# Performance work log

Measured on AMD Instinct MI355X. Metric: run time of the kernel, lower is better.

The kernel has to match this reference:

```python
import jax, jax.numpy as jnp
import numpy as np

STATE_DIM, ACTION_DIM, HIDDEN, ACTOR_HIDDEN = 64, 8, 256, 256
B, T = 1024, 512


def _uniform(key, shape, bound):
    return jax.random.uniform(key, shape, jnp.float32, -bound, bound)


def setup_inputs() -> dict:
    key = jax.random.key(0)
    ks = jax.random.split(key, 12)
    k = 1.0 / np.sqrt(HIDDEN)  # PyTorch GRU/Linear init bound
    ka = 1.0 / np.sqrt(ACTOR_HIDDEN)
    return {
        "x_seq": jax.random.normal(ks[0], (B, T, STATE_DIM), jnp.float32),
        # GRU params (PyTorch layout: [3*H, in] with gate order r,z,n)
        "w_ih": _uniform(ks[1], (3 * HIDDEN, STATE_DIM), k),
        "w_hh": _uniform(ks[2], (3 * HIDDEN, HIDDEN), k),
        "b_ih": _uniform(ks[3], (3 * HIDDEN,), k),
        "b_hh": _uniform(ks[4], (3 * HIDDEN,), k),
        # base MLP
        "w_base": _uniform(ks[5], (ACTOR_HIDDEN, HIDDEN), k),
        "b_base": _uniform(ks[6], (ACTOR_HIDDEN,), k),
        # factorized heads
        "w_dir": _uniform(ks[7], (ACTION_DIM, ACTOR_HIDDEN), ka),
        "b_dir": _uniform(ks[8], (ACTION_DIM,), ka),
        "w_mag": _uniform(ks[9], (ACTION_DIM, ACTOR_HIDDEN), ka),
        "b_mag": _uniform(ks[10], (ACTION_DIM,), ka),
    }


def reference(x_seq, w_ih, w_hh, b_ih, b_hh, w_base, b_base, w_dir, b_dir, w_mag, b_mag):
    H = w_hh.shape[1]

    def step(h, x_t):
        gi = x_t @ w_ih.T + b_ih          # [B, 3H]
        gh = h @ w_hh.T + b_hh            # [B, 3H]
        i_r, i_z, i_n = jnp.split(gi, 3, axis=-1)
        h_r, h_z, h_n = jnp.split(gh, 3, axis=-1)
        r = jax.nn.sigmoid(i_r + h_r)
        z = jax.nn.sigmoid(i_z + h_z)
        n = jnp.tanh(i_n + r * h_n)
        h_new = (1.0 - z) * n + z * h
        return h_new, None

    h0 = jnp.zeros((x_seq.shape[0], H), x_seq.dtype)
    last, _ = jax.lax.scan(step, h0, jnp.swapaxes(x_seq, 0, 1))  # carry = h_T
    h = jax.nn.relu(last @ w_base.T + b_base)
    direction = jnp.tanh(h @ w_dir.T + b_dir)
    magnitude = jax.nn.sigmoid(h @ w_mag.T + b_mag)
    return direction * magnitude
```

## Files before the change

### kernel.cpp

```cpp
#include <hip/hip_runtime.h>

#define T_SEQ 512
#define HID 256

typedef _Float16 half8 __attribute__((ext_vector_type(8)));
typedef _Float16 half4 __attribute__((ext_vector_type(4)));
typedef float floatx4 __attribute__((ext_vector_type(4)));

#define OFF_GH 0
#define OFF_GI (OFF_GH + 384 * 512)
#define OFF_WB (OFF_GI + 96 * 512)
#define OFF_WD (OFF_WB + 128 * 512)

#define MFMA16(A, B, C) __builtin_amdgcn_mfma_f32_16x16x32_f16(A, B, C, 0, 0, 0)

__device__ __forceinline__ float sigm(float x) { return 1.0f / (1.0f + __expf(-x)); }
__device__ __forceinline__ float tanh_fast(float x) {
  float e = __expf(2.0f * x);
  return 1.0f - 2.0f / (e + 1.0f);
}

__global__ void prep_kernel(const float* __restrict__ w_ih,
                            const float* __restrict__ w_hh,
                            const float* __restrict__ w_base,
                            const float* __restrict__ w_dir,
                            const float* __restrict__ w_mag,
                            _Float16* __restrict__ ws) {
  const int f = blockIdx.x;
  const int lane = threadIdx.x;
  const int col = lane & 15, quad = lane >> 4;
  const float* src;
  int n, k, ld;
  _Float16* dst;
  if (f < 384) {
    int nt = f % 6, kt = (f / 6) % 8, w = f / 48;
    n = (nt >> 1) * 256 + w * 32 + (nt & 1) * 16 + col;
    k = kt * 32 + quad * 8;
    src = w_hh; ld = 256;
    dst = ws + OFF_GH + ((w * 8 + kt) * 6 + nt) * 512 + lane * 8;
  } else if (f < 480) {
    int f2 = f - 384;
    int nt = f2 % 6, kt = (f2 / 6) % 2, w = f2 / 12;
    n = (nt >> 1) * 256 + w * 32 + (nt & 1) * 16 + col;
    k = kt * 32 + quad * 8;
    src = w_ih; ld = 64;
    dst = ws + OFF_GI + ((w * 2 + kt) * 6 + nt) * 512 + lane * 8;
  } else if (f < 608) {
    int f3 = f - 480;
    int nt = f3 % 2, kt = (f3 / 2) % 8, w = f3 / 16;
    n = w * 32 + nt * 16 + col;
    k = kt * 32 + quad * 8;
    src = w_base; ld = 256;
    dst = ws + OFF_WB + ((w * 8 + kt) * 2 + nt) * 512 + lane * 8;
  } else {
    int kt = f - 608;
    k = kt * 32 + quad * 8;
    ld = 256;
    if (col < 8) { src = w_dir; n = col; } else { src = w_mag; n = col - 8; }
    dst = ws + OFF_WD + kt * 512 + lane * 8;
  }
#pragma unroll
  for (int j = 0; j < 8; ++j)
    dst[j] = (_Float16)src[n * ld + k + j];
}

__global__ __launch_bounds__(512, 2)
void gru_head_kernel(const float* __restrict__ x_seq,
                     const float* __restrict__ b_ih,
                     const float* __restrict__ b_hh,
                     const float* __restrict__ b_base,
                     const float* __restrict__ b_dir,
                     const float* __restrict__ b_mag,
                     const _Float16* __restrict__ ws,
                     float* __restrict__ out) {
  __shared__ __align__(16) _Float16 hlin[2][4096];
  __shared__ __align__(16) _Float16 wlds[8][4096];

  const int tid = threadIdx.x;
  const int lane = tid & 63;
  const int w = tid >> 6;
  const int col = lane & 15;
  const int quad = lane >> 4;
  const int row0 = blockIdx.x * 16;

  *(half8*)&hlin[0][tid * 8] = (half8)((_Float16)0.0f);

  float br[2], bz[2], bin_[2], bhn[2];
#pragma unroll
  for (int s = 0; s < 2; ++s) {
    const int c = w * 32 + s * 16 + col;
    br[s] = b_ih[c] + b_hh[c];
    bz[s] = b_ih[256 + c] + b_hh[256 + c];
    bin_[s] = b_ih[512 + c];
    bhn[s] = b_hh[512 + c];
  }

  float hreg[2][4];
#pragma unroll
  for (int s = 0; s < 2; ++s)
#pragma unroll
    for (int r2 = 0; r2 < 4; ++r2) hreg[s][r2] = 0.0f;

  const half8* __restrict__ ghp = (const half8*)(ws + OFF_GH) + w * (48 * 64);
  const half8* __restrict__ gip = (const half8*)(ws + OFF_GI) + w * (12 * 64);
  const half8* __restrict__ wbp = (const half8*)(ws + OFF_WB) + w * (16 * 64);
  const half8* __restrict__ wdp = (const half8*)(ws + OFF_WD);

  half8 wreg[16];
#pragma unroll
  for (int f = 0; f < 16; ++f) wreg[f] = ghp[f * 64 + lane];
  _Float16* const wlw = wlds[w];
#pragma unroll
  for (int j = 0; j < 8; ++j)
    *(half8*)&wlw[j * 512 + lane * 8] = ghp[(16 + j) * 64 + lane];

  const float* const xlane = x_seq + ((size_t)(row0 + col) * T_SEQ) * 64 + quad * 8;

  float4 xc[4], xn[4];
  {
    const float* p = xlane;
    xc[0] = *(const float4*)(p);
    xc[1] = *(const float4*)(p + 4);
    xc[2] = *(const float4*)(p + 32);
    xc[3] = *(const float4*)(p + 36);
  }

  auto body = [&](int t, int tpre, int cur, float4* xcur, float4* xnext) {
    const int nxt = cur ^ 1;
    __syncthreads();

    half8 s1[6], s2[6];
#pragma unroll
    for (int i = 0; i < 6; ++i) s1[i] = ghp[(24 + i) * 64 + lane];
#pragma unroll
    for (int i = 0; i < 6; ++i) s2[i] = ghp[(30 + i) * 64 + lane];
    {
      const float* p = xlane + (size_t)tpre * 64;
      xnext[0] = *(const float4*)(p);
      xnext[1] = *(const float4*)(p + 4);
      xnext[2] = *(const float4*)(p + 32);
      xnext[3] = *(const float4*)(p + 36);
    }

    half8 ah[8];
#pragma unroll
    for (int kt = 0; kt < 8; ++kt)
      ah[kt] = *(const half8*)&hlin[cur][kt * 512 + lane * 8];
    half8 wl[8];
#pragma unroll
    for (int j = 0; j < 8; ++j)
      wl[j] = *(const half8*)&wlw[j * 512 + lane * 8];

    half8 ax0, ax1;
#pragma unroll
    for (int j = 0; j < 4; ++j) {
      ax0[j]     = (_Float16)((const float*)&xcur[0])[j];
      ax0[4 + j] = (_Float16)((const float*)&xcur[1])[j];
      ax1[j]     = (_Float16)((const float*)&xcur[2])[j];
      ax1[4 + j] = (_Float16)((const float*)&xcur[3])[j];
    }

    floatx4 acc[8];
#pragma unroll
    for (int i = 0; i < 8; ++i) acc[i] = (floatx4){0.f, 0.f, 0.f, 0.f};

#pragma unroll
    for (int f = 0; f < 16; ++f)
      acc[f % 6] = MFMA16(ah[f / 6], wreg[f], acc[f % 6]);

    half8 s3[6];
#pragma unroll
    for (int i = 0; i < 6; ++i) s3[i] = ghp[(36 + i) * 64 + lane];

#pragma unroll
    for (int j = 0; j < 8; ++j) {
      const int f = 16 + j;
      acc[f % 6] = MFMA16(ah[f / 6], wl[j], acc[f % 6]);
    }

#pragma unroll
    for (int i = 0; i < 6; ++i) {
      const int f = 24 + i;
      acc[f % 6] = MFMA16(ah[f / 6], s1[i], acc[f % 6]);
    }

    half8 s4[6];
#pragma unroll
    for (int i = 0; i < 6; ++i) s4[i] = ghp[(42 + i) * 64 + lane];

#pragma unroll
    for (int i = 0; i < 6; ++i) {
      const int f = 30 + i;
      acc[f % 6] = MFMA16(ah[f / 6], s2[i], acc[f % 6]);
    }

    half8 s5[6];
#pragma unroll
    for (int i = 0; i < 6; ++i) s5[i] = gip[i * 64 + lane];

#pragma unroll
    for (int i = 0; i < 6; ++i) {
      const int f = 36 + i;
      acc[f % 6] = MFMA16(ah[f / 6], s3[i], acc[f % 6]);
    }

    half8 s6[6];
#pragma unroll
    for (int i = 0; i < 6; ++i) s6[i] = gip[(6 + i) * 64 + lane];

#pragma unroll
    for (int i = 0; i < 6; ++i) {
      const int f = 42 + i;
      acc[f % 6] = MFMA16(ah[f / 6], s4[i], acc[f % 6]);
    }

#pragma unroll
    for (int i = 0; i < 6; ++i) {
      const int aidx = (i < 4) ? i : i + 2;
      acc[aidx] = MFMA16(ax0, s5[i], acc[aidx]);
    }
#pragma unroll
    for (int i = 0; i < 6; ++i) {
      const int aidx = (i < 4) ? i : i + 2;
      acc[aidx] = MFMA16(ax1, s6[i], acc[aidx]);
    }

#pragma unroll
    for (int s = 0; s < 2; ++s) {
      const int inner = s * 16 + col;
      const int widx = w * 512 + (inner >> 3) * 128 + (col & 7);
#pragma unroll
      for (int r2 = 0; r2 < 4; ++r2) {
        const int rw = quad * 4 + r2;
        const float rr = sigm(acc[0 + s][r2] + br[s]);
        const float zz = sigm(acc[2 + s][r2] + bz[s]);
        const float nn = tanh_fast(acc[6 + s][r2] + bin_[s] + rr * (acc[4 + s][r2] + bhn[s]));
        const float hnew = zz * hreg[s][r2] + (1.0f - zz) * nn;
        hreg[s][r2] = hnew;
        hlin[nxt][widx + rw * 8] = (_Float16)hnew;
      }
    }
  };

#pragma unroll 1
  for (int t = 0; t < T_SEQ; t += 2) {
    body(t, t + 1, 0, xc, xn);
    const int tp2 = (t + 2 < T_SEQ) ? (t + 2) : (T_SEQ - 1);
    body(t + 1, tp2, 1, xn, xc);
  }

  __syncthreads();
  {
    floatx4 ab[2];
    ab[0] = (floatx4){0.f, 0.f, 0.f, 0.f};
    ab[1] = (floatx4){0.f, 0.f, 0.f, 0.f};
#pragma unroll
    for (int kt = 0; kt < 8; ++kt) {
      const half8 ahh = *(const half8*)&hlin[0][kt * 512 + lane * 8];
      const half8* bp = wbp + kt * (2 * 64) + lane;
      ab[0] = MFMA16(ahh, bp[0],  ab[0]);
      ab[1] = MFMA16(ahh, bp[64], ab[1]);
    }
#pragma unroll
    for (int s = 0; s < 2; ++s) {
      const int inner = s * 16 + col;
      const int widx = w * 512 + (inner >> 3) * 128 + (col & 7);
      const float bb = b_base[w * 32 + inner];
#pragma unroll
      for (int r2 = 0; r2 < 4; ++r2) {
        const float v = ab[s][r2] + bb;
        hlin[1][widx + (quad * 4 + r2) * 8] = (_Float16)fmaxf(v, 0.0f);
      }
    }
  }
  __syncthreads();

  if (w == 0) {
    floatx4 ad = (floatx4){0.f, 0.f, 0.f, 0.f};
#pragma unroll
    for (int kt = 0; kt < 8; ++kt) {
      const half8 ahh = *(const half8*)&hlin[1][kt * 512 + lane * 8];
      ad = MFMA16(ahh, wdp[kt * 64 + lane], ad);
    }
    const float bd = (col < 8) ? b_dir[col] : b_mag[col - 8];
#pragma unroll
    for (int r2 = 0; r2 < 4; ++r2) {
      const float v = ad[r2] + bd;
      const float act = (col < 8) ? tanh_fast(v) : sigm(v);
      const float other = __shfl_xor(act, 8, 64);
      if (col < 8)
        out[(size_t)(row0 + quad * 4 + r2) * 8 + col] = act * other;
    }
  }
}

extern "C" void kernel_launch(void* const* d_in, const int* in_sizes, int n_in,
                              void* d_out, int out_size, void* d_ws, size_t ws_size,
                              hipStream_t stream) {
  const float* x_seq  = (const float*)d_in[0];
  const float* w_ih   = (const float*)d_in[1];
  const float* w_hh   = (const float*)d_in[2];
  const float* b_ih   = (const float*)d_in[3];
  const float* b_hh   = (const float*)d_in[4];
  const float* w_base = (const float*)d_in[5];
  const float* b_base = (const float*)d_in[6];
  const float* w_dir  = (const float*)d_in[7];
  const float* b_dir  = (const float*)d_in[8];
  const float* w_mag  = (const float*)d_in[9];
  const float* b_mag  = (const float*)d_in[10];
  _Float16* ws = (_Float16*)d_ws;
  float* out = (float*)d_out;

  hipLaunchKernelGGL(prep_kernel, dim3(616), dim3(64), 0, stream,
                     w_ih, w_hh, w_base, w_dir, w_mag, ws);
  hipLaunchKernelGGL(gru_head_kernel, dim3(64), dim3(512), 0, stream,
                     x_seq, b_ih, b_hh, b_base, b_dir, b_mag, ws, out);
}
```

Baseline: 2.187 ms.

## Precompute input-gate projections in parallel prepass, leaving recurrence with only hidden GEMM

Adds a separate kernel that computes x_t @ W_ih^T plus the folded biases for every timestep across 256 blocks, storing the results as fp16 in a large workspace region. The sequential recurrent kernel then loads these precomputed gate inputs per step instead of loading x and running 12 extra MFMAs, which shortens the serial critical path. It also drops the LDS-resident W_hh slice and streams those weights from global/L2 instead. The trade-off is roughly 200MB of extra fp16 traffic (written once, read once), extra fp16 rounding of the gate inputs, and a fallback path when the workspace is too small.

```diff
diff --git a/kernel.cpp b/kernel.cpp
--- a/kernel.cpp
+++ b/kernel.cpp
@@ -11,6 +11,11 @@
 #define OFF_GI (OFF_GH + 384 * 512)
 #define OFF_WB (OFF_GI + 96 * 512)
 #define OFF_WD (OFF_WB + 128 * 512)
+
+#define GI_OFF_BYTES (4ull << 20)
+#define GI_T_STRIDE 3072ull
+#define GI_B_STRIDE (512ull * 3072ull)
+#define WS_NEED (GI_OFF_BYTES + 64ull * GI_B_STRIDE * 8ull)
 
 #define MFMA16(A, B, C) __builtin_amdgcn_mfma_f32_16x16x32_f16(A, B, C, 0, 0, 0)
 
@@ -64,17 +69,96 @@
     dst[j] = (_Float16)src[n * ld + k + j];
 }
 
+__global__ __launch_bounds__(512, 1)
+void gi_prepass_kernel(const float* __restrict__ x_seq,
+                       const float* __restrict__ b_ih,
+                       const float* __restrict__ b_hh,
+                       const _Float16* __restrict__ ws,
+                       uint2* __restrict__ gi_out) {
+  const int tid = threadIdx.x;
+  const int lane = tid & 63;
+  const int w = tid >> 6;
+  const int col = lane & 15;
+  const int quad = lane >> 4;
+  const int btile = blockIdx.x >> 2, tq = blockIdx.x & 3;
+  const int row0 = btile * 16;
+
+  const half8* __restrict__ gip = (const half8*)(ws + OFF_GI) + w * (12 * 64);
+  half8 wg[12];
+#pragma unroll
+  for (int f = 0; f < 12; ++f) wg[f] = gip[f * 64 + lane];
+
+  float bias[6];
+#pragma unroll
+  for (int a = 0; a < 6; ++a) {
+    const int c = w * 32 + (a & 1) * 16 + col;
+    const int g = a >> 1;
+    bias[a] = (g < 2) ? (b_ih[g * 256 + c] + b_hh[g * 256 + c]) : b_ih[512 + c];
+  }
+
+  const float* const xlane = x_seq + (size_t)(row0 + col) * (T_SEQ * 64) + quad * 8;
+  uint2* const gout = gi_out + (size_t)btile * GI_B_STRIDE + (size_t)w * 384 + lane;
+
+  float4 xc[4], xn[4];
+  {
+    const float* p = xlane + (size_t)(tq * 128) * 64;
+    xc[0] = *(const float4*)(p);
+    xc[1] = *(const float4*)(p + 4);
+    xc[2] = *(const float4*)(p + 32);
+    xc[3] = *(const float4*)(p + 36);
+  }
+
+#pragma unroll 1
+  for (int tt = 0; tt < 128; ++tt) {
+    const int t = tq * 128 + tt;
+    if (tt + 1 < 128) {
+      const float* p = xlane + (size_t)(t + 1) * 64;
+      xn[0] = *(const float4*)(p);
+      xn[1] = *(const float4*)(p + 4);
+      xn[2] = *(const float4*)(p + 32);
+      xn[3] = *(const float4*)(p + 36);
+    }
+    half8 ax0, ax1;
+#pragma unroll
+    for (int j = 0; j < 4; ++j) {
+      ax0[j]     = (_Float16)((const float*)&xc[0])[j];
+      ax0[4 + j] = (_Float16)((const float*)&xc[1])[j];
+      ax1[j]     = (_Float16)((const float*)&xc[2])[j];
+      ax1[4 + j] = (_Float16)((const float*)&xc[3])[j];
+    }
+
+    floatx4 acc[6];
+#pragma unroll
+    for (int a = 0; a < 6; ++a) acc[a] = (floatx4){0.f, 0.f, 0.f, 0.f};
+#pragma unroll
+    for (int nt = 0; nt < 6; ++nt) {
+      acc[nt] = MFMA16(ax0, wg[nt], acc[nt]);
+      acc[nt] = MFMA16(ax1, wg[6 + nt], acc[nt]);
+    }
+
+    uint2* gp = gout + (size_t)t * GI_T_STRIDE;
+#pragma unroll
+    for (int a = 0; a < 6; ++a) {
+      union { uint2 u; half4 h; } pk;
+#pragma unroll
+      for (int r2 = 0; r2 < 4; ++r2)
+        pk.h[r2] = (_Float16)(acc[a][r2] + bias[a]);
+      gp[a * 64] = pk.u;
+    }
+#pragma unroll
+    for (int i = 0; i < 4; ++i) xc[i] = xn[i];
+  }
+}
+
 __global__ __launch_bounds__(512, 2)
-void gru_head_kernel(const float* __restrict__ x_seq,
-                     const float* __restrict__ b_ih,
-                     const float* __restrict__ b_hh,
+void gru_main_kernel(const float* __restrict__ b_hh,
                      const float* __restrict__ b_base,
                      const float* __restrict__ b_dir,
                      const float* __restrict__ b_mag,
                      const _Float16* __restrict__ ws,
+                     const uint2* __restrict__ gi_in,
                      float* __restrict__ out) {
   __shared__ __align__(16) _Float16 hlin[2][4096];
-  __shared__ __align__(16) _Float16 wlds[8][4096];
 
   const int tid = threadIdx.x;
   const int lane = tid & 63;
@@ -85,6 +169,172 @@
 
   *(half8*)&hlin[0][tid * 8] = (half8)((_Float16)0.0f);
 
+  float bhn[2];
+#pragma unroll
+  for (int s = 0; s < 2; ++s) bhn[s] = b_hh[512 + w * 32 + s * 16 + col];
+
+  float hreg[2][4];
+#pragma unroll
+  for (int s = 0; s < 2; ++s)
+#pragma unroll
+    for (int r2 = 0; r2 < 4; ++r2) hreg[s][r2] = 0.0f;
+
+  const half8* __restrict__ ghp = (const half8*)(ws + OFF_GH) + w * (48 * 64);
+  const half8* __restrict__ wbp = (const half8*)(ws + OFF_WB) + w * (16 * 64);
+  const half8* __restrict__ wdp = (const half8*)(ws + OFF_WD);
+
+  half8 wreg[16];
+#pragma unroll
+  for (int f = 0; f < 16; ++f) wreg[f] = ghp[f * 64 + lane];
+
+  const uint2* const gilane =
+      gi_in + (size_t)blockIdx.x * GI_B_STRIDE + (size_t)w * 384 + lane;
+
+#pragma unroll 1
+  for (int t = 0; t < T_SEQ; ++t) {
+    __syncthreads();
+    const int cur = t & 1;
+    const _Float16* hc = hlin[cur];
+    _Float16* hn = hlin[cur ^ 1];
+
+    uint2 g[6];
+    const uint2* gp = gilane + (size_t)t * GI_T_STRIDE;
+#pragma unroll
+    for (int a = 0; a < 6; ++a) g[a] = gp[a * 64];
+
+    half8 s1[8], s2[8];
+#pragma unroll
+    for (int i = 0; i < 8; ++i) s1[i] = ghp[(16 + i) * 64 + lane];
+#pragma unroll
+    for (int i = 0; i < 8; ++i) s2[i] = ghp[(24 + i) * 64 + lane];
+
+    half8 ah[8];
+#pragma unroll
+    for (int kt = 0; kt < 8; ++kt)
+      ah[kt] = *(const half8*)&hc[kt * 512 + lane * 8];
+
+    floatx4 acc[6];
+#pragma unroll
+    for (int a = 0; a < 6; ++a) acc[a] = (floatx4){0.f, 0.f, 0.f, 0.f};
+
+#pragma unroll
+    for (int f = 0; f < 16; ++f)
+      acc[f % 6] = MFMA16(ah[f / 6], wreg[f], acc[f % 6]);
+
+    half8 s3[8];
+#pragma unroll
+    for (int i = 0; i < 8; ++i) s3[i] = ghp[(32 + i) * 64 + lane];
+
+#pragma unroll
+    for (int i = 0; i < 8; ++i) {
+      const int f = 16 + i;
+      acc[f % 6] = MFMA16(ah[f / 6], s1[i], acc[f % 6]);
+    }
+
+    half8 s4[8];
+#pragma unroll
+    for (int i = 0; i < 8; ++i) s4[i] = ghp[(40 + i) * 64 + lane];
+
+#pragma unroll
+    for (int i = 0; i < 8; ++i) {
+      const int f = 24 + i;
+      acc[f % 6] = MFMA16(ah[f / 6], s2[i], acc[f % 6]);
+    }
+#pragma unroll
+    for (int i = 0; i < 8; ++i) {
+      const int f = 32 + i;
+      acc[f % 6] = MFMA16(ah[f / 6], s3[i], acc[f % 6]);
+    }
+#pragma unroll
+    for (int i = 0; i < 8; ++i) {
+      const int f = 40 + i;
+      acc[f % 6] = MFMA16(ah[f / 6], s4[i], acc[f % 6]);
+    }
+
+#pragma unroll
+    for (int s = 0; s < 2; ++s) {
+      const int inner = s * 16 + col;
+      const int widx = w * 512 + (inner >> 3) * 128 + (col & 7);
+      union { uint2 u; half4 h; } gr, gz, gn;
+      gr.u = g[0 + s]; gz.u = g[2 + s]; gn.u = g[4 + s];
+#pragma unroll
+      for (int r2 = 0; r2 < 4; ++r2) {
+        const float rr = sigm(acc[0 + s][r2] + (float)gr.h[r2]);
+        const float zz = sigm(acc[2 + s][r2] + (float)gz.h[r2]);
+        const float nn = tanh_fast((float)gn.h[r2] + rr * (acc[4 + s][r2] + bhn[s]));
+        const float hnew = zz * hreg[s][r2] + (1.0f - zz) * nn;
+        hreg[s][r2] = hnew;
+        hn[widx + (quad * 4 + r2) * 8] = (_Float16)hnew;
+      }
+    }
+  }
+
+  __syncthreads();
+  {
+    floatx4 ab[2];
+    ab[0] = (floatx4){0.f, 0.f, 0.f, 0.f};
+    ab[1] = (floatx4){0.f, 0.f, 0.f, 0.f};
+#pragma unroll
+    for (int kt = 0; kt < 8; ++kt) {
+      const half8 ahh = *(const half8*)&hlin[0][kt * 512 + lane * 8];
+      const half8* bp = wbp + kt * (2 * 64) + lane;
+      ab[0] = MFMA16(ahh, bp[0],  ab[0]);
+      ab[1] = MFMA16(ahh, bp[64], ab[1]);
+    }
+#pragma unroll
+    for (int s = 0; s < 2; ++s) {
+      const int inner = s * 16 + col;
+      const int widx = w * 512 + (inner >> 3) * 128 + (col & 7);
+      const float bb = b_base[w * 32 + inner];
+#pragma unroll
+      for (int r2 = 0; r2 < 4; ++r2) {
+        const float v = ab[s][r2] + bb;
+        hlin[1][widx + (quad * 4 + r2) * 8] = (_Float16)fmaxf(v, 0.0f);
+      }
+    }
+  }
+  __syncthreads();
+
+  if (w == 0) {
+    floatx4 ad = (floatx4){0.f, 0.f, 0.f, 0.f};
+#pragma unroll
+    for (int kt = 0; kt < 8; ++kt) {
+      const half8 ahh = *(const half8*)&hlin[1][kt * 512 + lane * 8];
+      ad = MFMA16(ahh, wdp[kt * 64 + lane], ad);
+    }
+    const float bd = (col < 8) ? b_dir[col] : b_mag[col - 8];
+#pragma unroll
+    for (int r2 = 0; r2 < 4; ++r2) {
+      const float v = ad[r2] + bd;
+      const float act = (col < 8) ? tanh_fast(v) : sigm(v);
+      const float other = __shfl_xor(act, 8, 64);
+      if (col < 8)
+        out[(size_t)(row0 + quad * 4 + r2) * 8 + col] = act * other;
+    }
+  }
+}
+
+__global__ __launch_bounds__(512, 2)
+void gru_head_fallback(const float* __restrict__ x_seq,
+                       const float* __restrict__ b_ih,
+                       const float* __restrict__ b_hh,
+                       const float* __restrict__ b_base,
+                       const float* __restrict__ b_dir,
+                       const float* __restrict__ b_mag,
+                       const _Float16* __restrict__ ws,
+                       float* __restrict__ out) {
+  __shared__ __align__(16) _Float16 hlin[2][4096];
+  __shared__ __align__(16) _Float16 wlds[8][4096];
+
+  const int tid = threadIdx.x;
+  const int lane = tid & 63;
+  const int w = tid >> 6;
+  const int col = lane & 15;
+  const int quad = lane >> 4;
+  const int row0 = blockIdx.x * 16;
+
+  *(half8*)&hlin[0][tid * 8] = (half8)((_Float16)0.0f);
+
   float br[2], bz[2], bin_[2], bhn[2];
 #pragma unroll
   for (int s = 0; s < 2; ++s) {
@@ -94,7 +344,6 @@
     bin_[s] = b_ih[512 + c];
     bhn[s] = b_hh[512 + c];
   }
-
   float hreg[2][4];
 #pragma unroll
   for (int s = 0; s < 2; ++s)
@@ -115,7 +364,6 @@
     *(half8*)&wlw[j * 512 + lane * 8] = ghp[(16 + j) * 64 + lane];
 
   const float* const xlane = x_seq + ((size_t)(row0 + col) * T_SEQ) * 64 + quad * 8;
-
   float4 xc[4], xn[4];
   {
     const float* p = xlane;
@@ -128,7 +376,6 @@
   auto body = [&](int t, int tpre, int cur, float4* xcur, float4* xnext) {
     const int nxt = cur ^ 1;
     __syncthreads();
-
     half8 s1[6], s2[6];
 #pragma unroll
     for (int i = 0; i < 6; ++i) s1[i] = ghp[(24 + i) * 64 + lane];
@@ -141,7 +388,6 @@
       xnext[2] = *(const float4*)(p + 32);
       xnext[3] = *(const float4*)(p + 36);
     }
-
     half8 ah[8];
 #pragma unroll
     for (int kt = 0; kt < 8; ++kt)
@@ -150,7 +396,6 @@
 #pragma unroll
     for (int j = 0; j < 8; ++j)
       wl[j] = *(const half8*)&wlw[j * 512 + lane * 8];
-
     half8 ax0, ax1;
 #pragma unroll
     for (int j = 0; j < 4; ++j) {
@@ -159,61 +404,49 @@
       ax1[j]     = (_Float16)((const float*)&xcur[2])[j];
       ax1[4 + j] = (_Float16)((const float*)&xcur[3])[j];
     }
-
     floatx4 acc[8];
 #pragma unroll
     for (int i = 0; i < 8; ++i) acc[i] = (floatx4){0.f, 0.f, 0.f, 0.f};
-
 #pragma unroll
     for (int f = 0; f < 16; ++f)
       acc[f % 6] = MFMA16(ah[f / 6], wreg[f], acc[f % 6]);
-
     half8 s3[6];
 #pragma unroll
     for (int i = 0; i < 6; ++i) s3[i] = ghp[(36 + i) * 64 + lane];
-
 #pragma unroll
     for (int j = 0; j < 8; ++j) {
       const int f = 16 + j;
       acc[f % 6] = MFMA16(ah[f / 6], wl[j], acc[f % 6]);
     }
-
 #pragma unroll
     for (int i = 0; i < 6; ++i) {
       const int f = 24 + i;
       acc[f % 6] = MFMA16(ah[f / 6], s1[i], acc[f % 6]);
     }
-
     half8 s4[6];
 #pragma unroll
     for (int i = 0; i < 6; ++i) s4[i] = ghp[(42 + i) * 64 + lane];
-
 #pragma unroll
     for (int i = 0; i < 6; ++i) {
       const int f = 30 + i;
       acc[f % 6] = MFMA16(ah[f / 6], s2[i], acc[f % 6]);
     }
-
     half8 s5[6];
 #pragma unroll
     for (int i = 0; i < 6; ++i) s5[i] = gip[i * 64 + lane];
-
 #pragma unroll
     for (int i = 0; i < 6; ++i) {
       const int f = 36 + i;
       acc[f % 6] = MFMA16(ah[f / 6], s3[i], acc[f % 6]);
     }
-
     half8 s6[6];
 #pragma unroll
     for (int i = 0; i < 6; ++i) s6[i] = gip[(6 + i) * 64 + lane];
-
 #pragma unroll
     for (int i = 0; i < 6; ++i) {
       const int f = 42 + i;
       acc[f % 6] = MFMA16(ah[f / 6], s4[i], acc[f % 6]);
     }
-
 #pragma unroll
     for (int i = 0; i < 6; ++i) {
       const int aidx = (i < 4) ? i : i + 2;
@@ -224,20 +457,18 @@
       const int aidx = (i < 4) ? i : i + 2;
       acc[aidx] = MFMA16(ax1, s6[i], acc[aidx]);
     }
-
 #pragma unroll
     for (int s = 0; s < 2; ++s) {
       const int inner = s * 16 + col;
       const int widx = w * 512 + (inner >> 3) * 128 + (col & 7);
 #pragma unroll
       for (int r2 = 0; r2 < 4; ++r2) {
-        const int rw = quad * 4 + r2;
         const float rr = sigm(acc[0 + s][r2] + br[s]);
         const float zz = sigm(acc[2 + s][r2] + bz[s]);
         const float nn = tanh_fast(acc[6 + s][r2] + bin_[s] + rr * (acc[4 + s][r2] + bhn[s]));
         const float hnew = zz * hreg[s][r2] + (1.0f - zz) * nn;
         hreg[s][r2] = hnew;
-        hlin[nxt][widx + rw * 8] = (_Float16)hnew;
+        hlin[nxt][widx + (quad * 4 + r2) * 8] = (_Float16)hnew;
       }
     }
   };
@@ -274,7 +505,6 @@
     }
   }
   __syncthreads();
-
   if (w == 0) {
     floatx4 ad = (floatx4){0.f, 0.f, 0.f, 0.f};
 #pragma unroll
@@ -298,21 +528,27 @@
                               void* d_out, int out_size, void* d_ws, size_t ws_size,
                               hipStream_t stream) {
   const float* x_seq  = (const float*)d_in[0];
-  const float* w_ih   = (const float*)d_in[1];
-  const float* w_hh   = (const float*)d_in[2];
   const float* b_ih   = (const float*)d_in[3];
   const float* b_hh   = (const float*)d_in[4];
-  const float* w_base = (const float*)d_in[5];
   const float* b_base = (const float*)d_in[6];
-  const float* w_dir  = (const float*)d_in[7];
   const float* b_dir  = (const float*)d_in[8];
-  const float* w_mag  = (const float*)d_in[9];
   const float* b_mag  = (const float*)d_in[10];
   _Float16* ws = (_Float16*)d_ws;
   float* out = (float*)d_out;
 
   hipLaunchKernelGGL(prep_kernel, dim3(616), dim3(64), 0, stream,
-                     w_ih, w_hh, w_base, w_dir, w_mag, ws);
-  hipLaunchKernelGGL(gru_head_kernel, dim3(64), dim3(512), 0, stream,
-                     x_seq, b_ih, b_hh, b_base, b_dir, b_mag, ws, out);
+                     (const float*)d_in[1], (const float*)d_in[2],
+                     (const float*)d_in[5], (const float*)d_in[7],
+                     (const float*)d_in[9], ws);
+
+  if (ws_size >= WS_NEED) {
+    uint2* gi = (uint2*)((char*)d_ws + GI_OFF_BYTES);
+    hipLaunchKernelGGL(gi_prepass_kernel, dim3(256), dim3(512), 0, stream,
+                       x_seq, b_ih, b_hh, ws, gi);
+    hipLaunchKernelGGL(gru_main_kernel, dim3(64), dim3(512), 0, stream,
+                       b_hh, b_base, b_dir, b_mag, ws, gi, out);
+  } else {
+    hipLaunchKernelGGL(gru_head_fallback, dim3(64), dim3(512), 0, stream,
+                       x_seq, b_ih, b_hh, b_base, b_dir, b_mag, ws, out);
+  }
 }
```

New measurement: 2.197 ms. No clear change (+0.4%).

## Split GRU work over 16 waves so all recurrent weights stay in registers

Applied to the files above, without the earlier changes.

Doubles the block to 1024 threads (16 waves), with each wave owning 16 hidden columns instead of 32. Each wave now holds its whole slice of W_hh (24 half8 fragments) in registers and keeps its W_ih slice in LDS. This removes the per-step global/L2 reloads of W_hh fragments and halves per-wave MFMA and elementwise work on the serial critical path. In exchange there are more waves per barrier, and the per-thread register budget is tighter under launch_bounds(1024,1).

```diff
diff --git a/kernel.cpp b/kernel.cpp
--- a/kernel.cpp
+++ b/kernel.cpp
@@ -64,7 +64,7 @@
     dst[j] = (_Float16)src[n * ld + k + j];
 }
 
-__global__ __launch_bounds__(512, 2)
+__global__ __launch_bounds__(1024, 1)
 void gru_head_kernel(const float* __restrict__ x_seq,
                      const float* __restrict__ b_ih,
                      const float* __restrict__ b_hh,
@@ -74,7 +74,7 @@
                      const _Float16* __restrict__ ws,
                      float* __restrict__ out) {
   __shared__ __align__(16) _Float16 hlin[2][4096];
-  __shared__ __align__(16) _Float16 wlds[8][4096];
+  __shared__ __align__(16) _Float16 wgi[16][6 * 512];
 
   const int tid = threadIdx.x;
   const int lane = tid & 63;
@@ -82,39 +82,42 @@
   const int col = lane & 15;
   const int quad = lane >> 4;
   const int row0 = blockIdx.x * 16;
-
-  *(half8*)&hlin[0][tid * 8] = (half8)((_Float16)0.0f);
-
-  float br[2], bz[2], bin_[2], bhn[2];
-#pragma unroll
-  for (int s = 0; s < 2; ++s) {
-    const int c = w * 32 + s * 16 + col;
-    br[s] = b_ih[c] + b_hh[c];
-    bz[s] = b_ih[256 + c] + b_hh[256 + c];
-    bin_[s] = b_ih[512 + c];
-    bhn[s] = b_hh[512 + c];
-  }
-
-  float hreg[2][4];
-#pragma unroll
-  for (int s = 0; s < 2; ++s)
-#pragma unroll
-    for (int r2 = 0; r2 < 4; ++r2) hreg[s][r2] = 0.0f;
-
-  const half8* __restrict__ ghp = (const half8*)(ws + OFF_GH) + w * (48 * 64);
-  const half8* __restrict__ gip = (const half8*)(ws + OFF_GI) + w * (12 * 64);
-  const half8* __restrict__ wbp = (const half8*)(ws + OFF_WB) + w * (16 * 64);
-  const half8* __restrict__ wdp = (const half8*)(ws + OFF_WD);
-
-  half8 wreg[16];
-#pragma unroll
-  for (int f = 0; f < 16; ++f) wreg[f] = ghp[f * 64 + lane];
-  _Float16* const wlw = wlds[w];
-#pragma unroll
-  for (int j = 0; j < 8; ++j)
-    *(half8*)&wlw[j * 512 + lane * 8] = ghp[(16 + j) * 64 + lane];
-
-  const float* const xlane = x_seq + ((size_t)(row0 + col) * T_SEQ) * 64 + quad * 8;
+  const int w8 = w >> 1, s = w & 1;
+
+  if (tid < 512) *(half8*)&hlin[0][tid * 8] = (half8)((_Float16)0.0f);
+
+  {
+    const half8* gip = (const half8*)(ws + OFF_GI) + w8 * (12 * 64);
+#pragma unroll
+    for (int g = 0; g < 3; ++g)
+#pragma unroll
+      for (int kt = 0; kt < 2; ++kt) {
+        const half8 v = gip[(kt * 6 + g * 2 + s) * 64 + lane];
+        *(half8*)&wgi[w][(g * 2 + kt) * 512 + lane * 8] = v;
+      }
+  }
+
+  const int c = w * 16 + col;
+  const float br = b_ih[c] + b_hh[c];
+  const float bz = b_ih[256 + c] + b_hh[256 + c];
+  const float bin_ = b_ih[512 + c];
+  const float bhn = b_hh[512 + c];
+
+  float hreg[4];
+#pragma unroll
+  for (int r2 = 0; r2 < 4; ++r2) hreg[r2] = 0.0f;
+
+  const half8* __restrict__ ghp = (const half8*)(ws + OFF_GH) + w8 * (48 * 64);
+  half8 wreg[24];
+#pragma unroll
+  for (int kt = 0; kt < 8; ++kt)
+#pragma unroll
+    for (int g = 0; g < 3; ++g)
+      wreg[kt * 3 + g] = ghp[(kt * 6 + g * 2 + s) * 64 + lane];
+
+  const float* const xlane = x_seq + (size_t)(row0 + col) * (T_SEQ * 64) + quad * 8;
+
+  const int widx = w8 * 512 + ((s * 16 + col) >> 3) * 128 + (col & 7);
 
   float4 xc[4], xn[4];
   {
@@ -126,14 +129,9 @@
   }
 
   auto body = [&](int t, int tpre, int cur, float4* xcur, float4* xnext) {
+    __syncthreads();
     const int nxt = cur ^ 1;
-    __syncthreads();
-
-    half8 s1[6], s2[6];
-#pragma unroll
-    for (int i = 0; i < 6; ++i) s1[i] = ghp[(24 + i) * 64 + lane];
-#pragma unroll
-    for (int i = 0; i < 6; ++i) s2[i] = ghp[(30 + i) * 64 + lane];
+
     {
       const float* p = xlane + (size_t)tpre * 64;
       xnext[0] = *(const float4*)(p);
@@ -146,10 +144,10 @@
 #pragma unroll
     for (int kt = 0; kt < 8; ++kt)
       ah[kt] = *(const half8*)&hlin[cur][kt * 512 + lane * 8];
-    half8 wl[8];
-#pragma unroll
-    for (int j = 0; j < 8; ++j)
-      wl[j] = *(const half8*)&wlw[j * 512 + lane * 8];
+    half8 wg[6];
+#pragma unroll
+    for (int j = 0; j < 6; ++j)
+      wg[j] = *(const half8*)&wgi[w][j * 512 + lane * 8];
 
     half8 ax0, ax1;
 #pragma unroll
@@ -160,85 +158,31 @@
       ax1[4 + j] = (_Float16)((const float*)&xcur[3])[j];
     }
 
-    floatx4 acc[8];
-#pragma unroll
-    for (int i = 0; i < 8; ++i) acc[i] = (floatx4){0.f, 0.f, 0.f, 0.f};
-
-#pragma unroll
-    for (int f = 0; f < 16; ++f)
-      acc[f % 6] = MFMA16(ah[f / 6], wreg[f], acc[f % 6]);
-
-    half8 s3[6];
-#pragma unroll
-    for (int i = 0; i < 6; ++i) s3[i] = ghp[(36 + i) * 64 + lane];
-
-#pragma unroll
-    for (int j = 0; j < 8; ++j) {
-      const int f = 16 + j;
-      acc[f % 6] = MFMA16(ah[f / 6], wl[j], acc[f % 6]);
-    }
-
-#pragma unroll
-    for (int i = 0; i < 6; ++i) {
-      const int f = 24 + i;
-      acc[f % 6] = MFMA16(ah[f / 6], s1[i], acc[f % 6]);
-    }
-
-    half8 s4[6];
-#pragma unroll
-    for (int i = 0; i < 6; ++i) s4[i] = ghp[(42 + i) * 64 + lane];
-
-#pragma unroll
-    for (int i = 0; i < 6; ++i) {
-      const int f = 30 + i;
-      acc[f % 6] = MFMA16(ah[f / 6], s2[i], acc[f % 6]);
-    }
-
-    half8 s5[6];
-#pragma unroll
-    for (int i = 0; i < 6; ++i) s5[i] = gip[i * 64 + lane];
-
-#pragma unroll
-    for (int i = 0; i < 6; ++i) {
-      const int f = 36 + i;
-      acc[f % 6] = MFMA16(ah[f / 6], s3[i], acc[f % 6]);
-    }
-
-    half8 s6[6];
-#pragma unroll
-    for (int i = 0; i < 6; ++i) s6[i] = gip[(6 + i) * 64 + lane];
-
-#pragma unroll
-    for (int i = 0; i < 6; ++i) {
-      const int f = 42 + i;
-      acc[f % 6] = MFMA16(ah[f / 6], s4[i], acc[f % 6]);
-    }
-
-#pragma unroll
-    for (int i = 0; i < 6; ++i) {
-      const int aidx = (i < 4) ? i : i + 2;
-      acc[aidx] = MFMA16(ax0, s5[i], acc[aidx]);
-    }
-#pragma unroll
-    for (int i = 0; i < 6; ++i) {
-      const int aidx = (i < 4) ? i : i + 2;
-      acc[aidx] = MFMA16(ax1, s6[i], acc[aidx]);
-    }
-
-#pragma unroll
-    for (int s = 0; s < 2; ++s) {
-      const int inner = s * 16 + col;
-      const int widx = w * 512 + (inner >> 3) * 128 + (col & 7);
-#pragma unroll
-      for (int r2 = 0; r2 < 4; ++r2) {
-        const int rw = quad * 4 + r2;
-        const float rr = sigm(acc[0 + s][r2] + br[s]);
-        const float zz = sigm(acc[2 + s][r2] + bz[s]);
-        const float nn = tanh_fast(acc[6 + s][r2] + bin_[s] + rr * (acc[4 + s][r2] + bhn[s]));
-        const float hnew = zz * hreg[s][r2] + (1.0f - zz) * nn;
-        hreg[s][r2] = hnew;
-        hlin[nxt][widx + rw * 8] = (_Float16)hnew;
-      }
+    floatx4 acc[4];
+#pragma unroll
+    for (int a = 0; a < 4; ++a) acc[a] = (floatx4){0.f, 0.f, 0.f, 0.f};
+
+#pragma unroll
+    for (int kt = 0; kt < 8; ++kt) {
+      acc[0] = MFMA16(ah[kt], wreg[kt * 3 + 0], acc[0]);
+      acc[1] = MFMA16(ah[kt], wreg[kt * 3 + 1], acc[1]);
+      acc[2] = MFMA16(ah[kt], wreg[kt * 3 + 2], acc[2]);
+    }
+    acc[0] = MFMA16(ax0, wg[0], acc[0]);
+    acc[0] = MFMA16(ax1, wg[1], acc[0]);
+    acc[1] = MFMA16(ax0, wg[2], acc[1]);
+    acc[1] = MFMA16(ax1, wg[3], acc[1]);
+    acc[3] = MFMA16(ax0, wg[4], acc[3]);
+    acc[3] = MFMA16(ax1, wg[5], acc[3]);
+
+#pragma unroll
+    for (int r2 = 0; r2 < 4; ++r2) {
+      const float rr = sigm(acc[0][r2] + br);
+      const float zz = sigm(acc[1][r2] + bz);
+      const float nn = tanh_fast(acc[3][r2] + bin_ + rr * (acc[2][r2] + bhn));
+      const float hnew = zz * hreg[r2] + (1.0f - zz) * nn;
+      hreg[r2] = hnew;
+      hlin[nxt][widx + (quad * 4 + r2) * 8] = (_Float16)hnew;
     }
   };
 
@@ -251,31 +195,25 @@
 
   __syncthreads();
   {
-    floatx4 ab[2];
-    ab[0] = (floatx4){0.f, 0.f, 0.f, 0.f};
-    ab[1] = (floatx4){0.f, 0.f, 0.f, 0.f};
+    const half8* wbp = (const half8*)(ws + OFF_WB) + (w8 * 16 + s) * 64;
+    floatx4 ab = (floatx4){0.f, 0.f, 0.f, 0.f};
 #pragma unroll
     for (int kt = 0; kt < 8; ++kt) {
       const half8 ahh = *(const half8*)&hlin[0][kt * 512 + lane * 8];
-      const half8* bp = wbp + kt * (2 * 64) + lane;
-      ab[0] = MFMA16(ahh, bp[0],  ab[0]);
-      ab[1] = MFMA16(ahh, bp[64], ab[1]);
-    }
-#pragma unroll
-    for (int s = 0; s < 2; ++s) {
-      const int inner = s * 16 + col;
-      const int widx = w * 512 + (inner >> 3) * 128 + (col & 7);
-      const float bb = b_base[w * 32 + inner];
-#pragma unroll
-      for (int r2 = 0; r2 < 4; ++r2) {
-        const float v = ab[s][r2] + bb;
-        hlin[1][widx + (quad * 4 + r2) * 8] = (_Float16)fmaxf(v, 0.0f);
-      }
+      ab = MFMA16(ahh, wbp[kt * 128 + lane], ab);
+    }
+    const float bb = b_base[c];
+    __syncthreads();
+#pragma unroll
+    for (int r2 = 0; r2 < 4; ++r2) {
+      const float v = ab[r2] + bb;
+      hlin[1][widx + (quad * 4 + r2) * 8] = (_Float16)fmaxf(v, 0.0f);
     }
   }
   __syncthreads();
 
   if (w == 0) {
+    const half8* wdp = (const half8*)(ws + OFF_WD);
     floatx4 ad = (floatx4){0.f, 0.f, 0.f, 0.f};
 #pragma unroll
     for (int kt = 0; kt < 8; ++kt) {
@@ -298,21 +236,18 @@
                               void* d_out, int out_size, void* d_ws, size_t ws_size,
                               hipStream_t stream) {
   const float* x_seq  = (const float*)d_in[0];
-  const float* w_ih   = (const float*)d_in[1];
-  const float* w_hh   = (const float*)d_in[2];
   const float* b_ih   = (const float*)d_in[3];
   const float* b_hh   = (const float*)d_in[4];
-  const float* w_base = (const float*)d_in[5];
   const float* b_base = (const float*)d_in[6];
-  const float* w_dir  = (const float*)d_in[7];
   const float* b_dir  = (const float*)d_in[8];
-  const float* w_mag  = (const float*)d_in[9];
   const float* b_mag  = (const float*)d_in[10];
   _Float16* ws = (_Float16*)d_ws;
   float* out = (float*)d_out;
 
   hipLaunchKernelGGL(prep_kernel, dim3(616), dim3(64), 0, stream,
-                     w_ih, w_hh, w_base, w_dir, w_mag, ws);
-  hipLaunchKernelGGL(gru_head_kernel, dim3(64), dim3(512), 0, stream,
+                     (const float*)d_in[1], (const float*)d_in[2],
+                     (const float*)d_in[5], (const float*)d_in[7],
+                     (const float*)d_in[9], ws);
+  hipLaunchKernelGGL(gru_head_kernel, dim3(64), dim3(1024), 0, stream,
                      x_seq, b_ih, b_hh, b_base, b_dir, b_mag, ws, out);
 }
```

Result: slower. 3.721 ms (+70.1%).
